# Kernel tuning notes

Hardware: AMD Instinct MI355X
Metric: run time of the kernel (lower is better)

The kernel has to match this reference:

```python
import jax, jax.numpy as jnp
import numpy as np
import math

HIDDEN = 2048
HEADS = 16
G = 4          # kv groups (= self.num_group after the module's head_num//num_group)
HPG = HEADS // G  # q heads per group
D = HIDDEN // HEADS  # 128


def setup_inputs() -> dict:
    key = jax.random.key(0)
    ks = jax.random.split(key, 9)
    B, S = 2, 2048
    s = 0.02
    return {
        "x": jax.random.normal(ks[0], (B, S, HIDDEN), dtype=jnp.float32),
        "Wq": jax.random.normal(ks[1], (HIDDEN, HIDDEN), dtype=jnp.float32) * s,
        "bq": jnp.zeros((HIDDEN,), jnp.float32),
        "Wk": jax.random.normal(ks[2], (HIDDEN, G * D), dtype=jnp.float32) * s,
        "bk": jnp.zeros((G * D,), jnp.float32),
        "Wv": jax.random.normal(ks[3], (HIDDEN, G * D), dtype=jnp.float32) * s,
        "bv": jnp.zeros((G * D,), jnp.float32),
        "Wo": jax.random.normal(ks[4], (HIDDEN, HIDDEN), dtype=jnp.float32) * s,
        "bo": jnpp if False else jnp.zeros((HIDDEN,), jnp.float32),
    }


def reference(x, Wq, bq, Wk, bk, Wv, bv, Wo, bo):
    B, S, H = x.shape
    # projections (torch Linear with W stored as (in, out))
    q = (x @ Wq + bq).reshape(B, S, G, HPG, D)   # (B,S,G,Hpg,D)
    k = (x @ Wk + bk).reshape(B, S, G, D)        # (B,S,G,D)
    v = (x @ Wv + bv).reshape(B, S, G, D)
    scale = 1.0 / math.sqrt(D)
    # scores: each of the Hpg query heads in a group shares the group's K/V
    scores = jnp.einsum("bsghd,btgd->bghst", q, k) * scale  # (B,G,Hpg,S,S)
    attn = jax.nn.softmax(scores, axis=-1)
    # dropout is identity in eval mode
    o = jnp.einsum("bghst,btgd->bsghd", attn, v).reshape(B, S, H)
    return o @ Wo + bo
```

## Files before the change

### kernel.cpp

```cpp
#include <hip/hip_runtime.h>

#define HID   2048
#define KD    2048
#define GQ    4
#define HPGQ  4
#define DH    128
#define SEQ   2048
#define NBATCH 2
#define NTOK  (NBATCH * SEQ)
#define NQKV  3072

typedef unsigned short u16;
typedef unsigned int   u32;
using bf16x8 = __attribute__((ext_vector_type(8))) __bf16;
using bf16x2 = __attribute__((ext_vector_type(2))) __bf16;
using f32x4  = __attribute__((ext_vector_type(4))) float;
using u32x4  = __attribute__((ext_vector_type(4))) u32;

#if __has_builtin(__builtin_amdgcn_exp2f)
#define FEXP2(x) __builtin_amdgcn_exp2f(x)
#else
#define FEXP2(x) exp2f(x)
#endif

#define QSCALE 0.12751744f

__device__ __forceinline__ u16 f2bf(float f) {
  union { float f; u32 u; } v; v.f = f;
  u32 u = v.u + 0x7fffu + ((v.u >> 16) & 1u);
  return (u16)(u >> 16);
}

__device__ __forceinline__ u32 pk2(float a, float b) {
  bf16x2 t;
  t[0] = (__bf16)a;
  t[1] = (__bf16)b;
  return __builtin_bit_cast(u32, t);
}

__device__ __forceinline__ void gl16(const void* g, void* l) {
  __builtin_amdgcn_global_load_lds((const __attribute__((address_space(1))) u32*)g,
                                   (__attribute__((address_space(3))) u32*)l, 16, 0, 0);
}

__device__ __forceinline__ int swz(int r, int c) {
  return (c & ~7) | ((c ^ r ^ (r >> 3)) & 7);
}

__global__ __launch_bounds__(256) void k_cvt_bf16(const float* __restrict__ in,
                                                  u16* __restrict__ out, int n4) {
  int i = blockIdx.x * 256 + threadIdx.x;
  if (i < n4) {
    const float4 v = ((const float4*)in)[i];
    ushort4 o;
    o.x = f2bf(v.x); o.y = f2bf(v.y); o.z = f2bf(v.z); o.w = f2bf(v.w);
    ((ushort4*)out)[i] = o;
  }
}

__global__ __launch_bounds__(256) void k_trans_all(
    const float* __restrict__ Wq, const float* __restrict__ Wk,
    const float* __restrict__ Wv, const float* __restrict__ Wo,
    u16* __restrict__ qkvT, u16* __restrict__ WoT) {
  __shared__ float tile[32][33];
  const int z = blockIdx.z;
  const float* W = (z == 0) ? Wq : (z == 1) ? Wk : (z == 2) ? Wv : Wo;
  u16* WT = (z == 3) ? WoT : qkvT;
  const int N = (z == 1 || z == 2) ? 512 : 2048;
  const int rowoff = (z == 1) ? 2048 : (z == 2) ? 2560 : 0;
  const int n0 = blockIdx.x * 32;
  if (n0 >= N) return;
  const int tx = threadIdx.x, ty = threadIdx.y;
  const int k0 = blockIdx.y * 32;
#pragma unroll
  for (int i = 0; i < 4; ++i)
    tile[ty + 8 * i][tx] = W[(size_t)(k0 + ty + 8 * i) * N + (n0 + tx)];
  __syncthreads();
#pragma unroll
  for (int i = 0; i < 4; ++i)
    WT[(size_t)(rowoff + n0 + ty + 8 * i) * KD + (k0 + tx)] = f2bf(tile[tx][ty + 8 * i]);
}


#define QBUF 114688
#define BUFB 57344

#define STG128(OP, ROWB, KTB, LBYTE)                                               \
  { _Pragma("unroll") for (int i = 0; i < 2; ++i)                                  \
      gl16((OP) + (size_t)(ROWB) * KD + (KTB) + stOffE[i],                         \
           (u16*)((char*)S + (LBYTE)) + (i * 512 + t) * 8); }
#define STG64(OP, ROWB, KTB, LBYTE)                                                \
  gl16((OP) + (size_t)(ROWB) * KD + (KTB) + stOffE[0],                             \
       (u16*)((char*)S + (LBYTE)) + t * 8);

#define STAGE_B(D, KTB)                                                            \
  STG128(Bt, n0b,       (KTB), (D) * BUFB + 32768);                                \
  STG64 (Bt, n0b + 128, (KTB), (D) * BUFB + 49152);
#define STAGE_A(D, KTB)                                                            \
  STG128(A,  m0,        (KTB), (D) * BUFB + 0);                                    \
  STG128(A,  m0 + 128,  (KTB), (D) * BUFB + 16384);

#define RDA(D, M, KC) (*(const bf16x8*)((const char*)S + (D) * BUFB + (M) * 2048 + (aQ ^ ((KC) << 6))))
#define RDB(D, NT, KC) (*(const bf16x8*)((const char*)S + (D) * BUFB + (NT) * 2048 + (bQ ^ ((KC) << 6))))

#define MFMA8(MB, NT)                                                              \
  _Pragma("unroll") for (int m = 0; m < 4; ++m)                                    \
    _Pragma("unroll") for (int kc = 0; kc < 2; ++kc)                               \
      acc[(MB) + m][NT] = __builtin_amdgcn_mfma_f32_16x16x32_bf16(                 \
          afr[m][kc], bfr[NT][kc], acc[(MB) + m][NT], 0, 0, 0);

#define ITERQ(D, KTN, PRE)                                                         \
  do {                                                                             \
                                                                           \
    _Pragma("unroll") for (int m = 0; m < 4; ++m)                                  \
      _Pragma("unroll") for (int kc = 0; kc < 2; ++kc)                             \
        afr[m][kc] = RDA(D, m, kc);                                                \
    _Pragma("unroll") for (int nt = 0; nt < 2; ++nt)                               \
      _Pragma("unroll") for (int kc = 0; kc < 2; ++kc)                             \
        bfr[nt][kc] = RDB(D, nt, kc);                                              \
    asm volatile("s_waitcnt lgkmcnt(8)" ::: "memory");                             \
    __builtin_amdgcn_s_barrier();                                                  \
    __builtin_amdgcn_s_setprio(1);                                                 \
    MFMA8(0, 0) MFMA8(0, 1)                                                        \
    __builtin_amdgcn_s_setprio(0);                                                 \
    __builtin_amdgcn_s_barrier();                                                  \
                                                                           \
    _Pragma("unroll") for (int kc = 0; kc < 2; ++kc)                               \
      bfr[2][kc] = RDB(D, 2, kc);                                                  \
    __builtin_amdgcn_s_barrier();                                                  \
    __builtin_amdgcn_s_setprio(1);                                                 \
    MFMA8(0, 2)                                                                    \
    __builtin_amdgcn_s_setprio(0);                                                 \
    __builtin_amdgcn_s_barrier();                                                  \
                                                                           \
    _Pragma("unroll") for (int m = 0; m < 4; ++m)                                  \
      _Pragma("unroll") for (int kc = 0; kc < 2; ++kc)                             \
        afr[m][kc] = RDA(D, 4 + m, kc);                                            \
    if (PRE) { STAGE_B(D, KTN); }                                                  \
    __builtin_amdgcn_s_barrier();                                                  \
    __builtin_amdgcn_s_setprio(1);                                                 \
    MFMA8(4, 2)                                                                    \
    __builtin_amdgcn_s_setprio(0);                                                 \
    __builtin_amdgcn_s_barrier();                                                  \
                                                                           \
    if (PRE) {                                                                     \
      STAGE_A(D, KTN);                                                             \
      asm volatile("s_waitcnt vmcnt(7)" ::: "memory");                             \
    } else {                                                                       \
      asm volatile("s_waitcnt vmcnt(0)" ::: "memory");                             \
    }                                                                              \
    __builtin_amdgcn_s_barrier();                                                  \
    __builtin_amdgcn_s_setprio(1);                                                 \
    MFMA8(4, 0) MFMA8(4, 1)                                                        \
    __builtin_amdgcn_s_setprio(0);                                                 \
    __builtin_amdgcn_s_barrier();                                                  \
  } while (0)

__global__ __launch_bounds__(512, 1) void k_gemm_qkv(
    const u16* __restrict__ A, const u16* __restrict__ Bt,
    u16* __restrict__ qkv, u16* __restrict__ vT,
    const float* __restrict__ bq, const float* __restrict__ bk,
    const float* __restrict__ bv) {
  __shared__ u16 S[QBUF / 2];
  const int t = threadIdx.x, l = t & 63, w = t >> 6;
  const int lr = l & 15, lk = l >> 4;
  const int wm = w >> 2, wn = w & 3;
  const int m0 = blockIdx.y * 256, n0b = blockIdx.x * 192;

  int stOffE[2];
#pragma unroll
  for (int i = 0; i < 2; ++i) {
    const int e = i * 512 + t;
    const int r = e >> 3;
    stOffE[i] = r * KD + ((e & 7) ^ (r & 7)) * 8;
  }
  const int qb = lr * 128 + (((lr >> 2) & 1) << 6) + ((lk ^ (lr & 3)) << 4);
  const int aQ = wm * 16384 + qb;
  const int bQ = 32768 + wn * 6144 + qb;

  f32x4 acc[8][3] = {};
  bf16x8 afr[4][2], bfr[3][2];

  STAGE_A(0, 0);  STAGE_B(0, 0);
  STAGE_A(1, 64); STAGE_B(1, 64);
  asm volatile("s_waitcnt vmcnt(7)" ::: "memory");
  __builtin_amdgcn_s_barrier();

  for (int j = 0; j < 30; j += 2) {
    ITERQ(0, (j + 2) * 64, true);
    ITERQ(1, (j + 3) * 64, true);
  }
  ITERQ(0, 0, false);
  ITERQ(1, 0, false);

  const int gmB = m0 + wm * 128, gnB = n0b + wn * 48;
#pragma unroll
  for (int m = 0; m < 8; ++m) {
    const int row0 = gmB + m * 16 + lk * 4;
#pragma unroll
    for (int nt = 0; nt < 3; ++nt) {
      const int col = gnB + nt * 16 + lr;
      float bias, qs = 1.0f;
      if (col < HID) { bias = bq[col]; qs = QSCALE; }
      else if (col < HID + 512) bias = bk[col - HID];
      else bias = bv[col - HID - 512];
      if (col < HID + 512) {
#pragma unroll
        for (int r = 0; r < 4; ++r)
          qkv[(size_t)(row0 + r) * NQKV + col] = f2bf((acc[m][nt][r] + bias) * qs);
      } else {
        const int gg = (col - 2560) >> 7, d = (col - 2560) & 127;
        const int b = row0 >> 11, s0 = row0 & 2047;
        ushort4 pk;
        pk.x = f2bf(acc[m][nt][0] + bias);
        pk.y = f2bf(acc[m][nt][1] + bias);
        pk.z = f2bf(acc[m][nt][2] + bias);
        pk.w = f2bf(acc[m][nt][3] + bias);
        *(ushort4*)(vT + ((size_t)(b * GQ + gg) * DH + d) * SEQ + s0) = pk;
      }
    }
  }
}

#define GEMM_STEP(CUR, NXT, K0N, PRE)                                              \
  do {                                                                             \
    if (PRE) {                                                                     \
      const u16* aB = A  + (size_t)m0 * KD + (K0N);                                \
      const u16* bB = Bt + (size_t)n0 * KD + (K0N);                                \
      _Pragma("unroll")                                                            \
      for (int i = 0; i < 2; ++i) {                                                \
        gl16(aB + stOff[i], So + (NXT)*4096 + (i * 256 + t) * 8);                  \
        gl16(bB + stOff[i], So + 8192 + (NXT)*4096 + (i * 256 + t) * 8);           \
      }                                                                            \
      asm volatile("s_waitcnt vmcnt(4)" ::: "memory");                             \
    } else {                                                                       \
      asm volatile("s_waitcnt vmcnt(0)" ::: "memory");                             \
    }                                                                              \
    __builtin_amdgcn_s_barrier();                                                  \
    bf16x8 af[4], bfr[4];                                                          \
    _Pragma("unroll")                                                              \
    for (int m = 0; m < 4; ++m)                                                    \
      af[m] = *(const bf16x8*)((const char*)So + (CUR)*8192 + m * 1024 + aAddr);   \
    _Pragma("unroll")                                                              \
    for (int n = 0; n < 4; ++n)                                                    \
      bfr[n] = *(const bf16x8*)((const char*)So + 16384 + (CUR)*8192 + n * 1024 + bAddr); \
    __builtin_amdgcn_s_setprio(1);                                                 \
    _Pragma("unroll")                                                              \
    for (int m = 0; m < 4; ++m)                                                    \
      _Pragma("unroll")                                                            \
      for (int n = 0; n < 4; ++n)                                                  \
        acc[m][n] = __builtin_amdgcn_mfma_f32_16x16x32_bf16(af[m], bfr[n], acc[m][n], 0, 0, 0); \
    __builtin_amdgcn_s_setprio(0);                                                 \
    __builtin_amdgcn_s_barrier();                                                  \
  } while (0)

__global__ __launch_bounds__(256) void k_gemm_o(
    const u16* __restrict__ A, const u16* __restrict__ Bt,
    const float* __restrict__ bo, float* __restrict__ C) {
  __shared__ u16 So[16384];
  const int t = threadIdx.x, l = t & 63, w = t >> 6;
  const int lr = l & 15, lk = l >> 4;
  const int wr = w >> 1, wc = w & 1;
  const int m0 = blockIdx.y * 128, n0 = blockIdx.x * 128;
  int stOff[2];
#pragma unroll
  for (int i = 0; i < 2; ++i) {
    const int e = i * 256 + t;
    const int r = e >> 2;
    const int cs = (e & 3) ^ ((r >> 1) & 3);
    stOff[i] = r * KD + cs * 8;
  }
  const int axor = (lk ^ ((lr >> 1) & 3)) << 4;
  const int aAddr = (wr * 64 + lr) * 64 + axor;
  const int bAddr = (wc * 64 + lr) * 64 + axor;
  f32x4 acc[4][4] = {};
  {
    const u16* aB = A  + (size_t)m0 * KD;
    const u16* bB = Bt + (size_t)n0 * KD;
#pragma unroll
    for (int i = 0; i < 2; ++i) {
      gl16(aB + stOff[i], So + (i * 256 + t) * 8);
      gl16(bB + stOff[i], So + 8192 + (i * 256 + t) * 8);
    }
  }
  for (int kt = 0; kt < KD / 32 - 2; kt += 2) {
    GEMM_STEP(0, 1, (kt + 1) * 32, true);
    GEMM_STEP(1, 0, (kt + 2) * 32, true);
  }
  GEMM_STEP(0, 1, (KD / 32 - 1) * 32, true);
  GEMM_STEP(1, 0, 0, false);

  const int gm = m0 + wr * 64, gn = n0 + wc * 64;
#pragma unroll
  for (int m = 0; m < 4; ++m) {
    const int row0 = gm + m * 16 + lk * 4;
#pragma unroll
    for (int n = 0; n < 4; ++n) {
      const int col = gn + n * 16 + lr;
      const float bias = bo[col];
#pragma unroll
      for (int r = 0; r < 4; ++r)
        C[(size_t)(row0 + r) * HID + col] = acc[m][n][r] + bias;
    }
  }
}

#define ATTN_ITER(KS, VS, KN, VN, TTV, PRE)                                        \
  do {                                                                             \
    if (PRE) {                                                                     \
      const int t0n = ((start + (TTV) + 1) & (NT - 1)) * 32;                       \
      const u16* kbT = kbase + (size_t)t0n * NQKV;                                 \
      const u16* vbT = vbase + t0n;                                                \
      _Pragma("unroll")                                                            \
      for (int i = 0; i < 2; ++i) {                                                \
        gl16(kbT + kOffE[i], (KN) + (i * 256 + t) * 8);                            \
        gl16(vbT + vOffE[i], (VN) + (i * 256 + t) * 8);                            \
      }                                                                            \
      asm volatile("s_waitcnt vmcnt(4)" ::: "memory");                             \
    } else {                                                                       \
      asm volatile("s_waitcnt vmcnt(0)" ::: "memory");                             \
    }                                                                              \
    __builtin_amdgcn_s_barrier();                                                  \
    f32x4 sc[2][2] = {};                                                           \
    __builtin_amdgcn_s_setprio(1);                                                 \
    _Pragma("unroll")                                                              \
    for (int kk = 0; kk < 4; ++kk) {                                               \
      bf16x8 kf[2];                                                                \
      _Pragma("unroll")                                                            \
      for (int mk = 0; mk < 2; ++mk) {                                             \
        const int LIT = (mk << 12) ^ ((kk >> 1) << 7) ^ ((kk & 1) << 6) ^ (mk << 5); \
        kf[mk] = *(const bf16x8*)((const char*)(KS) + (kQ0 ^ LIT));                \
      }                                                                            \
      _Pragma("unroll")                                                            \
      for (int nq = 0; nq < 2; ++nq)                                               \
        _Pragma("unroll")                                                          \
        for (int mk = 0; mk < 2; ++mk)                                             \
          sc[nq][mk] = __builtin_amdgcn_mfma_f32_16x16x32_bf16(kf[mk], qf[nq][kk], sc[nq][mk], 0, 0, 0); \
    }                                                                              \
    __builtin_amdgcn_s_setprio(0);                                                 \
    bf16x8 pa[2];                                                                  \
    _Pragma("unroll")                                                              \
    for (int nq = 0; nq < 2; ++nq) {                                               \
      u32 w0 = pk2(FEXP2(sc[nq][0][0]), FEXP2(sc[nq][0][1]));                      \
      u32 w1 = pk2(FEXP2(sc[nq][0][2]), FEXP2(sc[nq][0][3]));                      \
      u32 w2 = pk2(FEXP2(sc[nq][1][0]), FEXP2(sc[nq][1][1]));                      \
      u32 w3 = pk2(FEXP2(sc[nq][1][2]), FEXP2(sc[nq][1][3]));                      \
      asm("v_permlane32_swap_b32 %0, %1" : "+v"(w0), "+v"(w2));                    \
      asm("v_permlane32_swap_b32 %0, %1" : "+v"(w1), "+v"(w3));                    \
      asm("v_permlane16_swap_b32 %0, %1" : "+v"(w0), "+v"(w2));                    \
      asm("v_permlane16_swap_b32 %0, %1" : "+v"(w1), "+v"(w3));                    \
      u32x4 u = {w0, w1, w2, w3};                                                  \
      pa[nq] = __builtin_bit_cast(bf16x8, u);                                      \
    }                                                                              \
    __builtin_amdgcn_s_setprio(1);                                                 \
    _Pragma("unroll")                                                              \
    for (int nq = 0; nq < 2; ++nq)                                                 \
      acc_s[nq] = __builtin_amdgcn_mfma_f32_16x16x32_bf16(pa[nq], vones, acc_s[nq], 0, 0, 0); \
    _Pragma("unroll")                                                              \
    for (int nd = 0; nd < 8; ++nd) {                                               \
      const bf16x8 vf = *(const bf16x8*)((const char*)(VS) + vQ0 + nd * 1024);     \
      _Pragma("unroll")                                                            \
      for (int nq = 0; nq < 2; ++nq)                                               \
        acc_o[nq][nd] = __builtin_amdgcn_mfma_f32_16x16x32_bf16(pa[nq], vf, acc_o[nq][nd], 0, 0, 0); \
    }                                                                              \
    __builtin_amdgcn_s_setprio(0);                                                 \
    __builtin_amdgcn_s_barrier();                                                  \
  } while (0)

__global__ __launch_bounds__(256, 2) void k_attn(
    const u16* __restrict__ qkv, const u16* __restrict__ vT, u16* __restrict__ o_ws) {
  __shared__ u16 smem[16384];
  u16* const kb0 = smem;
  u16* const kb1 = smem + 4096;
  u16* const vb0 = smem + 8192;
  u16* const vb1 = smem + 12288;

  const int t = threadIdx.x, l = t & 63, w = t >> 6;
  const int lr = l & 15, lk = l >> 4;
  const int f = blockIdx.x;
  const int bg = f & 7;
  const int h = (f >> 3) & 3;
  const int qt = f >> 5;
  const int b = bg >> 2, g = bg & 3;
  const int q0 = qt * 128;
  const int qcol = (g * HPGQ + h) * DH;
  const u16* qbase = qkv + (size_t)(b * SEQ) * NQKV;
  const u16* kbase = qbase + HID + g * DH;
  const u16* vbase = vT + (size_t)(b * GQ + g) * DH * SEQ;

  const int NT = SEQ / 32;
  const int start = (qt * 5 + h * 9) & (NT - 1);

  const int kQ0 = lr * 256 + ((lk ^ (lr & 7) ^ (lr >> 3)) << 4);
  const int vQ0 = lr * 64 + ((lk ^ ((lr >> 1) & 3)) << 4);
  int kOffE[2], vOffE[2];
#pragma unroll
  for (int i = 0; i < 2; ++i) {
    const int e = i * 256 + t;
    const int r = e >> 4, c = e & 15;
    kOffE[i] = r * NQKV + swz(r, c) * 8;
    const int rv = e >> 2, cv = e & 3;
    vOffE[i] = rv * SEQ + ((cv ^ ((rv >> 1) & 3)) * 8);
  }

  bf16x8 qf[2][4];
#pragma unroll
  for (int nq = 0; nq < 2; ++nq)
#pragma unroll
    for (int kk = 0; kk < 4; ++kk)
      qf[nq][kk] = *(const bf16x8*)(qbase + (size_t)(q0 + w * 32 + nq * 16 + lr) * NQKV +
                                    qcol + kk * 32 + lk * 8);

  {
    const int t00 = start * 32;
    const u16* kbT = kbase + (size_t)t00 * NQKV;
    const u16* vbT = vbase + t00;
#pragma unroll
    for (int i = 0; i < 2; ++i) {
      gl16(kbT + kOffE[i], kb0 + (i * 256 + t) * 8);
      gl16(vbT + vOffE[i], vb0 + (i * 256 + t) * 8);
    }
  }

  f32x4 acc_o[2][8] = {};
  f32x4 acc_s[2] = {};

  bf16x8 vones;
#pragma unroll
  for (int j = 0; j < 8; ++j) vones[j] = (lr == 0) ? (__bf16)1.0f : (__bf16)0.0f;

  for (int tp = 0; tp < NT - 2; tp += 2) {
    ATTN_ITER(kb0, vb0, kb1, vb1, tp, true);
    ATTN_ITER(kb1, vb1, kb0, vb0, tp + 1, true);
  }
  ATTN_ITER(kb0, vb0, kb1, vb1, NT - 2, true);
  ATTN_ITER(kb1, vb1, kb0, vb0, NT - 1, false);

#pragma unroll
  for (int nq = 0; nq < 2; ++nq)
#pragma unroll
    for (int r = 0; r < 4; ++r) {
      const float s = __shfl(acc_s[nq][r], l & 48);
      const float inv = 1.0f / s;
      const int q = q0 + w * 32 + nq * 16 + lk * 4 + r;
#pragma unroll
      for (int nd = 0; nd < 8; ++nd) {
        const int d = nd * 16 + lr;
        o_ws[(size_t)(b * SEQ + q) * HID + qcol + d] = f2bf(acc_o[nq][nd][r] * inv);
      }
    }
}

extern "C" void kernel_launch(void* const* d_in, const int* in_sizes, int n_in,
                              void* d_out, int out_size, void* d_ws, size_t ws_size,
                              hipStream_t stream) {
  const float* x  = (const float*)d_in[0];
  const float* Wq = (const float*)d_in[1];
  const float* bq = (const float*)d_in[2];
  const float* Wk = (const float*)d_in[3];
  const float* bk = (const float*)d_in[4];
  const float* Wv = (const float*)d_in[5];
  const float* bv = (const float*)d_in[6];
  const float* Wo = (const float*)d_in[7];
  const float* bo = (const float*)d_in[8];
  float* out = (float*)d_out;

  char* ws = (char*)d_ws;
  u16* x_bf  = (u16*)ws;  ws += (size_t)NTOK * KD * 2;
  u16* qkvT  = (u16*)ws;  ws += (size_t)NQKV * KD * 2;
  u16* WoT   = (u16*)ws;  ws += (size_t)HID * KD * 2;
  u16* qkv   = (u16*)ws;  ws += (size_t)NTOK * NQKV * 2;
  u16* vTb   = (u16*)ws;  ws += (size_t)NBATCH * GQ * DH * SEQ * 2;
  u16* o_ws  = x_bf;

  k_cvt_bf16<<<(NTOK * KD / 4 + 255) / 256, 256, 0, stream>>>(x, x_bf, NTOK * KD / 4);
  k_trans_all<<<dim3(64, 64, 4), dim3(32, 8), 0, stream>>>(Wq, Wk, Wv, Wo, qkvT, WoT);

  k_gemm_qkv<<<dim3(NQKV / 192, NTOK / 256), 512, 0, stream>>>(x_bf, qkvT, qkv, vTb, bq, bk, bv);
  k_attn<<<SEQ / 128 * NBATCH * GQ * HPGQ, 256, 0, stream>>>(qkv, vTb, o_ws);
  k_gemm_o<<<dim3(HID / 128, NTOK / 128), 256, 0, stream>>>(o_ws, WoT, bo, out);
}
```

Before: 186.9 us.

## Restructure output projection GEMM into 256x128 tiles with interleaved staged pipeline

```diff
diff --git a/kernel.cpp b/kernel.cpp
--- a/kernel.cpp
+++ b/kernel.cpp
@@ -81,7 +81,6 @@
     WT[(size_t)(rowoff + n0 + ty + 8 * i) * KD + (k0 + tx)] = f2bf(tile[tx][ty + 8 * i]);
 }
 
-
 #define QBUF 114688
 #define BUFB 57344
 
@@ -222,85 +221,116 @@
   }
 }
 
-#define GEMM_STEP(CUR, NXT, K0N, PRE)                                              \
+
+#define OBUFB 49152
+
+#define OSTAGE_B(D, KTB)                                                           \
+  STG128(Bt, n0b, (KTB), (D) * OBUFB + 32768);
+#define OSTAGE_A(D, KTB)                                                           \
+  STG128(A,  m0,       (KTB), (D) * OBUFB + 0);                                    \
+  STG128(A,  m0 + 128, (KTB), (D) * OBUFB + 16384);
+
+#define ORDA(D, M, KC) (*(const bf16x8*)((const char*)S + (D) * OBUFB + (M) * 2048 + (aQ ^ ((KC) << 6))))
+#define ORDB(D, NT, KC) (*(const bf16x8*)((const char*)S + (D) * OBUFB + (NT) * 2048 + (bQ ^ ((KC) << 6))))
+
+#define OMFMA8(MB, NT)                                                             \
+  _Pragma("unroll") for (int m = 0; m < 4; ++m)                                    \
+    _Pragma("unroll") for (int kc = 0; kc < 2; ++kc)                               \
+      acc[(MB) + m][NT] = __builtin_amdgcn_mfma_f32_16x16x32_bf16(                 \
+          afr[m][kc], bfr[NT][kc], acc[(MB) + m][NT], 0, 0, 0);
+
+#define ITERO(D, KTN, PRE)                                                         \
   do {                                                                             \
+                                                                           \
+    _Pragma("unroll") for (int m = 0; m < 4; ++m)                                  \
+      _Pragma("unroll") for (int kc = 0; kc < 2; ++kc)                             \
+        afr[m][kc] = ORDA(D, m, kc);                                               \
+    _Pragma("unroll") for (int kc = 0; kc < 2; ++kc)                               \
+      bfr[0][kc] = ORDB(D, 0, kc);                                                 \
+    asm volatile("s_waitcnt lgkmcnt(8)" ::: "memory");                             \
+    __builtin_amdgcn_s_barrier();                                                  \
+    __builtin_amdgcn_s_setprio(1);                                                 \
+    OMFMA8(0, 0)                                                                   \
+    __builtin_amdgcn_s_setprio(0);                                                 \
+    __builtin_amdgcn_s_barrier();                                                  \
+                                                                           \
+    _Pragma("unroll") for (int kc = 0; kc < 2; ++kc)                               \
+      bfr[1][kc] = ORDB(D, 1, kc);                                                 \
+    __builtin_amdgcn_s_barrier();                                                  \
+    __builtin_amdgcn_s_setprio(1);                                                 \
+    OMFMA8(0, 1)                                                                   \
+    __builtin_amdgcn_s_setprio(0);                                                 \
+    __builtin_amdgcn_s_barrier();                                                  \
+                                                                           \
+    _Pragma("unroll") for (int m = 0; m < 4; ++m)                                  \
+      _Pragma("unroll") for (int kc = 0; kc < 2; ++kc)                             \
+        afr[m][kc] = ORDA(D, 4 + m, kc);                                           \
+    if (PRE) { OSTAGE_B(D, KTN); }                                                 \
+    __builtin_amdgcn_s_barrier();                                                  \
+    __builtin_amdgcn_s_setprio(1);                                                 \
+    OMFMA8(4, 1)                                                                   \
+    __builtin_amdgcn_s_setprio(0);                                                 \
+    __builtin_amdgcn_s_barrier();                                                  \
+                                                                           \
     if (PRE) {                                                                     \
-      const u16* aB = A  + (size_t)m0 * KD + (K0N);                                \
-      const u16* bB = Bt + (size_t)n0 * KD + (K0N);                                \
-      _Pragma("unroll")                                                            \
-      for (int i = 0; i < 2; ++i) {                                                \
-        gl16(aB + stOff[i], So + (NXT)*4096 + (i * 256 + t) * 8);                  \
-        gl16(bB + stOff[i], So + 8192 + (NXT)*4096 + (i * 256 + t) * 8);           \
-      }                                                                            \
-      asm volatile("s_waitcnt vmcnt(4)" ::: "memory");                             \
+      OSTAGE_A(D, KTN);                                                            \
+      asm volatile("s_waitcnt vmcnt(6)" ::: "memory");                             \
     } else {                                                                       \
       asm volatile("s_waitcnt vmcnt(0)" ::: "memory");                             \
     }                                                                              \
     __builtin_amdgcn_s_barrier();                                                  \
-    bf16x8 af[4], bfr[4];                                                          \
-    _Pragma("unroll")                                                              \
-    for (int m = 0; m < 4; ++m)                                                    \
-      af[m] = *(const bf16x8*)((const char*)So + (CUR)*8192 + m * 1024 + aAddr);   \
-    _Pragma("unroll")                                                              \
-    for (int n = 0; n < 4; ++n)                                                    \
-      bfr[n] = *(const bf16x8*)((const char*)So + 16384 + (CUR)*8192 + n * 1024 + bAddr); \
-    __builtin_amdgcn_s_setprio(1);                                                 \
-    _Pragma("unroll")                                                              \
-    for (int m = 0; m < 4; ++m)                                                    \
-      _Pragma("unroll")                                                            \
-      for (int n = 0; n < 4; ++n)                                                  \
-        acc[m][n] = __builtin_amdgcn_mfma_f32_16x16x32_bf16(af[m], bfr[n], acc[m][n], 0, 0, 0); \
+    __builtin_amdgcn_s_setprio(1);                                                 \
+    OMFMA8(4, 0)                                                                   \
     __builtin_amdgcn_s_setprio(0);                                                 \
     __builtin_amdgcn_s_barrier();                                                  \
   } while (0)
 
-__global__ __launch_bounds__(256) void k_gemm_o(
+__global__ __launch_bounds__(512, 1) void k_gemm_o(
     const u16* __restrict__ A, const u16* __restrict__ Bt,
     const float* __restrict__ bo, float* __restrict__ C) {
-  __shared__ u16 So[16384];
+  __shared__ u16 S[OBUFB];
   const int t = threadIdx.x, l = t & 63, w = t >> 6;
   const int lr = l & 15, lk = l >> 4;
-  const int wr = w >> 1, wc = w & 1;
-  const int m0 = blockIdx.y * 128, n0 = blockIdx.x * 128;
-  int stOff[2];
+  const int wm = w >> 2, wn = w & 3;
+  const int m0 = blockIdx.y * 256, n0b = blockIdx.x * 128;
+
+  int stOffE[2];
 #pragma unroll
   for (int i = 0; i < 2; ++i) {
-    const int e = i * 256 + t;
-    const int r = e >> 2;
-    const int cs = (e & 3) ^ ((r >> 1) & 3);
-    stOff[i] = r * KD + cs * 8;
-  }
-  const int axor = (lk ^ ((lr >> 1) & 3)) << 4;
-  const int aAddr = (wr * 64 + lr) * 64 + axor;
-  const int bAddr = (wc * 64 + lr) * 64 + axor;
-  f32x4 acc[4][4] = {};
-  {
-    const u16* aB = A  + (size_t)m0 * KD;
-    const u16* bB = Bt + (size_t)n0 * KD;
-#pragma unroll
-    for (int i = 0; i < 2; ++i) {
-      gl16(aB + stOff[i], So + (i * 256 + t) * 8);
-      gl16(bB + stOff[i], So + 8192 + (i * 256 + t) * 8);
-    }
-  }
-  for (int kt = 0; kt < KD / 32 - 2; kt += 2) {
-    GEMM_STEP(0, 1, (kt + 1) * 32, true);
-    GEMM_STEP(1, 0, (kt + 2) * 32, true);
-  }
-  GEMM_STEP(0, 1, (KD / 32 - 1) * 32, true);
-  GEMM_STEP(1, 0, 0, false);
-
-  const int gm = m0 + wr * 64, gn = n0 + wc * 64;
-#pragma unroll
-  for (int m = 0; m < 4; ++m) {
-    const int row0 = gm + m * 16 + lk * 4;
-#pragma unroll
-    for (int n = 0; n < 4; ++n) {
-      const int col = gn + n * 16 + lr;
+    const int e = i * 512 + t;
+    const int r = e >> 3;
+    stOffE[i] = r * KD + ((e & 7) ^ (r & 7)) * 8;
+  }
+  const int qb = lr * 128 + (((lr >> 2) & 1) << 6) + ((lk ^ (lr & 3)) << 4);
+  const int aQ = wm * 16384 + qb;
+  const int bQ = 32768 + wn * 4096 + qb;
+
+  f32x4 acc[8][2] = {};
+  bf16x8 afr[4][2], bfr[2][2];
+
+  OSTAGE_A(0, 0);  OSTAGE_B(0, 0);
+  OSTAGE_A(1, 64); OSTAGE_B(1, 64);
+  asm volatile("s_waitcnt vmcnt(6)" ::: "memory");
+  __builtin_amdgcn_s_barrier();
+
+  for (int j = 0; j < 30; j += 2) {
+    ITERO(0, (j + 2) * 64, true);
+    ITERO(1, (j + 3) * 64, true);
+  }
+  ITERO(0, 0, false);
+  ITERO(1, 0, false);
+
+  const int gmB = m0 + wm * 128, gnB = n0b + wn * 32;
+#pragma unroll
+  for (int m = 0; m < 8; ++m) {
+    const int row0 = gmB + m * 16 + lk * 4;
+#pragma unroll
+    for (int nt = 0; nt < 2; ++nt) {
+      const int col = gnB + nt * 16 + lr;
       const float bias = bo[col];
 #pragma unroll
       for (int r = 0; r < 4; ++r)
-        C[(size_t)(row0 + r) * HID + col] = acc[m][n][r] + bias;
+        C[(size_t)(row0 + r) * HID + col] = acc[m][nt][r] + bias;
     }
   }
 }
@@ -478,5 +508,5 @@
 
   k_gemm_qkv<<<dim3(NQKV / 192, NTOK / 256), 512, 0, stream>>>(x_bf, qkvT, qkv, vTb, bq, bk, bv);
   k_attn<<<SEQ / 128 * NBATCH * GQ * HPGQ, 256, 0, stream>>>(qkv, vTb, o_ws);
-  k_gemm_o<<<dim3(HID / 128, NTOK / 128), 256, 0, stream>>>(o_ws, WoT, bo, out);
-}
+  k_gemm_o<<<dim3(HID / 128, NTOK / 256), 512, 0, stream>>>(o_ws, WoT, bo, out);
+}
```

Result: no change. 183.4 us (-1.9%).
